# Kernel tuning notes

Measured on AMD Instinct MI355X. Metric: run time of the kernel, lower is better.

Reference implementation:

```python
import jax, jax.numpy as jnp
import numpy as np

N, E, D_IN, H, C, N_GRAPHS = 50000, 800000, 128, 2, 64, 50
D_HID = H * C  # 128
NEG_SLOPE = 0.2
EPS = 1e-16


def glorot(key, shape):
    fan_in, fan_out = shape[0], shape[-1]
    lim = jnp.sqrt(6.0 / (fan_in + fan_out))
    return jax.random.uniform(key, shape, jnp.float32, -lim, lim)


def setup_inputs() -> dict:
    key = jax.random.key(0)
    ks = jax.random.split(key, 12)
    x = jax.random.normal(ks[0], (N, D_IN), jnp.float32)
    edge_index = jax.random.randint(ks[1], (2, E), 0, N, jnp.int64)
    batch = jnp.sort(jax.random.randint(ks[2], (N,), 0, N_GRAPHS, jnp.int64))
    # GATConv layer 1: in=128 -> heads=2, out=64
    W1 = glorot(ks[3], (D_IN, H * C))
    as1 = glorot(ks[4], (1, H, C)).reshape(H, C)
    ad1 = glorot(ks[5], (1, H, C)).reshape(H, C)
    b1 = jnp.zeros((H * C,), jnp.float32)
    # GATConv layer 2: in=128 -> heads=2, out=64
    W2 = glorot(ks[6], (D_HID, H * C))
    as2 = glorot(ks[7], (1, H, C)).reshape(H, C)
    ad2 = glorot(ks[8], (1, H, C)).reshape(H, C)
    b2 = jnp.zeros((H * C,), jnp.float32)
    # Linear head: 128 -> 1
    Wh = glorot(ks[9], (D_HID, 1))
    bh = jnp.zeros((1,), jnp.float32)
    return {"x": x, "edge_index": edge_index, "batch": batch,
            "W1": W1, "as1": as1, "ad1": ad1, "b1": b1,
            "W2": W2, "as2": as2, "ad2": ad2, "b2": b2,
            "Wh": Wh, "bh": bh}


def gat_conv(x, src, dst, W, a_src, a_dst, bias):
    # PyG GATConv (concat=True, add_self_loops applied by caller, eval mode)
    n = x.shape[0]
    h = (x @ W).reshape(n, H, C)                       # [N,H,C]
    al_s = jnp.einsum('nhc,hc->nh', h, a_src)          # [N,H]
    al_d = jnp.einsum('nhc,hc->nh', h, a_dst)
    e = jax.nn.leaky_relu(al_s[src] + al_d[dst], NEG_SLOPE)  # [E',H]
    # segment softmax over incoming edges of each dst node
    e_max = jax.ops.segment_max(e, dst, num_segments=n)
    e = jnp.exp(e - e_max[dst])
    denom = jax.ops.segment_sum(e, dst, num_segments=n)
    alpha = e / (denom[dst] + EPS)                     # [E',H]
    out = jax.ops.segment_sum(alpha[:, :, None] * h[src], dst, num_segments=n)
    return out.reshape(n, H * C) + bias


def reference(x, edge_index, batch, W1, as1, ad1, b1, W2, as2, ad2, b2, Wh, bh):
    # add self-loops (PyG GATConv default)
    loops = jnp.arange(N, dtype=edge_index.dtype)
    src = jnp.concatenate([edge_index[0], loops])
    dst = jnp.concatenate([edge_index[1], loops])
    h = gat_conv(x, src, dst, W1, as1, ad1, b1)
    h = jax.nn.relu(h)  # dropout is identity in eval mode
    h = gat_conv(h, src, dst, W2, as2, ad2, b2)
    h = jax.nn.relu(h)
    # global mean pool over graphs
    sums = jax.ops.segment_sum(h, batch, num_segments=N_GRAPHS)
    counts = jax.ops.segment_sum(jnp.ones((N, 1), h.dtype), batch, num_segments=N_GRAPHS)
    pooled = sums / jnp.maximum(counts, 1.0)           # [G, 128]
    return pooled @ Wh + bh                            # [G, 1]
```

## Files before the change

### kernel.cpp

```cpp
#include <hip/hip_runtime.h>
#include <hip/hip_fp16.h>
#include <math.h>

#define HD 128
#define NEG_SLOPE 0.2f
#define EPSV 1e-16f
#define TILE 8192

typedef unsigned short ushort_t;
typedef __attribute__((ext_vector_type(8))) short bf16x8;
typedef __attribute__((ext_vector_type(4))) float f32x4;

__device__ inline void bsplit(float x, ushort_t& hi, ushort_t& lo) {
    unsigned u = __float_as_uint(x);
    unsigned hb = (u + 0x7FFFu + ((u >> 16) & 1u)) >> 16;
    hi = (ushort_t)hb;
    float res = x - __uint_as_float(hb << 16);
    unsigned v = __float_as_uint(res);
    lo = (ushort_t)((v + 0x7FFFu + ((v >> 16) & 1u)) >> 16);
}

__global__ __launch_bounds__(256) void part_hist(const int* __restrict__ dst,
                                                 int* __restrict__ tileHist, int E) {
    __shared__ int hist[256];
    int t = threadIdx.x;
    hist[t] = 0;
    __syncthreads();
    int base = blockIdx.x * TILE;
    int end = base + TILE; if (end > E) end = E;
    for (int i = base + t; i < end; i += 256)
        atomicAdd(&hist[dst[i] >> 8], 1);
    __syncthreads();
    tileHist[blockIdx.x * 256 + t] = hist[t];
}

__global__ __launch_bounds__(256) void part_offsets(int* __restrict__ tileHist,
                                                    int* __restrict__ bucketBase,
                                                    int NT) {
    __shared__ int s[256];
    int b = threadIdx.x;
    int total = 0;
    #pragma unroll 8
    for (int t = 0; t < NT; ++t) total += tileHist[t * 256 + b];
    s[b] = total;
    __syncthreads();
    for (int o = 1; o < 256; o <<= 1) {
        int v = (b >= o) ? s[b - o] : 0;
        __syncthreads();
        s[b] += v;
        __syncthreads();
    }
    int base = (b == 0) ? 0 : s[b - 1];
    bucketBase[b] = base;
    if (b == 255) bucketBase[256] = s[255];
    int run = base;
    #pragma unroll 8
    for (int t = 0; t < NT; ++t) {
        int v = tileHist[t * 256 + b];
        tileHist[t * 256 + b] = run;
        run += v;
    }
}

__global__ __launch_bounds__(256) void part_scatter(const int* __restrict__ src,
                                                    const int* __restrict__ dst,
                                                    const int* __restrict__ tileHist,
                                                    int2* __restrict__ part, int E) {
    __shared__ int cur[256];
    int t = threadIdx.x;
    cur[t] = tileHist[blockIdx.x * 256 + t];
    __syncthreads();
    int base = blockIdx.x * TILE;
    int end = base + TILE; if (end > E) end = E;
    for (int i = base + t; i < end; i += 256) {
        int d = dst[i], s = src[i];
        int p = atomicAdd(&cur[d >> 8], 1);
        part[p] = make_int2(s, d);
    }
}

__global__ __launch_bounds__(256) void fine_counts(const int2* __restrict__ part,
                                                   const int* __restrict__ bucketBase,
                                                   int* __restrict__ cnt, int N) {
    __shared__ int hist[256];
    int t = threadIdx.x;
    hist[t] = 0;
    __syncthreads();
    int b = blockIdx.x;
    int s0 = bucketBase[b], s1 = bucketBase[b + 1];
    for (int i = s0 + t; i < s1; i += 256)
        atomicAdd(&hist[part[i].y & 255], 1);
    __syncthreads();
    int d = b * 256 + t;
    if (d < N) cnt[d] = hist[t] + 1;
}

__global__ __launch_bounds__(256) void block_sums(const int* __restrict__ cnt,
                                                  int* __restrict__ bsum, int N) {
    __shared__ int s[4];
    int t = threadIdx.x;
    int i = blockIdx.x * 256 + t;
    int v = (i < N) ? cnt[i] : 0;
    for (int o = 32; o >= 1; o >>= 1) v += __shfl_xor(v, o, 64);
    if ((t & 63) == 0) s[t >> 6] = v;
    __syncthreads();
    if (t == 0) bsum[blockIdx.x] = s[0] + s[1] + s[2] + s[3];
}

__global__ __launch_bounds__(256) void scan_bsums(int* __restrict__ bsum, int NB) {
    __shared__ int s[256];
    __shared__ int carry;
    int t = threadIdx.x;
    if (t == 0) carry = 0;
    __syncthreads();
    for (int base = 0; base < NB; base += 256) {
        int i = base + t;
        int v = (i < NB) ? bsum[i] : 0;
        s[t] = v;
        __syncthreads();
        for (int o = 1; o < 256; o <<= 1) {
            int u = (t >= o) ? s[t - o] : 0;
            __syncthreads();
            s[t] += u;
            __syncthreads();
        }
        int excl = ((t == 0) ? 0 : s[t - 1]) + carry;
        if (i < NB) bsum[i] = excl;
        __syncthreads();
        if (t == 0) carry += s[255];
        __syncthreads();
    }
}

__global__ __launch_bounds__(256) void scatter_scan(const int* __restrict__ cnt,
                                                    const int* __restrict__ bsum,
                                                    int* __restrict__ indptr, int N) {
    __shared__ int s[256];
    int t = threadIdx.x;
    int i = blockIdx.x * 256 + t;
    int v = (i < N) ? cnt[i] : 0;
    s[t] = v;
    __syncthreads();
    for (int o = 1; o < 256; o <<= 1) {
        int u = (t >= o) ? s[t - o] : 0;
        __syncthreads();
        s[t] += u;
        __syncthreads();
    }
    int excl = ((t == 0) ? 0 : s[t - 1]) + bsum[blockIdx.x];
    if (i < N) indptr[i] = excl;
    if (i == N - 1) indptr[N] = excl + v;
}

__global__ __launch_bounds__(256) void csr_scatter(const int2* __restrict__ part,
                                                   const int* __restrict__ bucketBase,
                                                   const int* __restrict__ indptr,
                                                   int* __restrict__ csr, int N) {
    __shared__ int cur[256];
    int t = threadIdx.x;
    int b = blockIdx.x;
    int d = b * 256 + t;
    cur[t] = (d < N) ? indptr[d] : 0;
    __syncthreads();
    int s0 = bucketBase[b], s1 = bucketBase[b + 1];
    for (int i = s0 + t; i < s1; i += 256) {
        int2 e = part[i];
        int p = atomicAdd(&cur[e.y & 255], 1);
        csr[p] = e.x;
    }
    __syncthreads();
    if (d < N) csr[cur[t]] = d;
}

__global__ __launch_bounds__(256) void split_w(const float* __restrict__ W,
                                               ushort_t* __restrict__ Whs,
                                               ushort_t* __restrict__ Wls) {
    int idx = blockIdx.x * 256 + threadIdx.x;
    int j    = idx & 7;
    int lane = (idx >> 3) & 63;
    int ks   = (idx >> 9) & 3;
    int ct   = idx >> 11;
    int n = ct * 16 + (lane & 15);
    int k = ks * 32 + (lane >> 4) * 8 + j;
    ushort_t hi, lo;
    bsplit(W[k * 128 + n], hi, lo);
    Whs[idx] = hi;
    Wls[idx] = lo;
}

__device__ inline void load8(const float* p, float* vv) {
    float4 a = *(const float4*)p;
    float4 b = *(const float4*)(p + 4);
    vv[0]=a.x; vv[1]=a.y; vv[2]=a.z; vv[3]=a.w;
    vv[4]=b.x; vv[5]=b.y; vv[6]=b.z; vv[7]=b.w;
}
__device__ inline void load8(const __half* p, float* vv) {
    bf16x8 r = *(const bf16x8*)p;
    #pragma unroll
    for (int j = 0; j < 8; ++j)
        vv[j] = __half2float(__ushort_as_half((ushort_t)r[j]));
}

template <typename TA>
__global__ __launch_bounds__(256) void gemm_mfma(const TA* __restrict__ A,
                                                 const ushort_t* __restrict__ Whs,
                                                 const ushort_t* __restrict__ Wls,
                                                 const float* __restrict__ a_s,
                                                 const float* __restrict__ a_d,
                                                 __half* __restrict__ h16,
                                                 float* __restrict__ als,
                                                 float* __restrict__ ald, int N) {
    const int gw   = (blockIdx.x * 256 + threadIdx.x) >> 6;
    const int lane = threadIdx.x & 63;
    const int r0   = gw * 16;
    if (r0 >= N) return;
    const int m = lane & 15;
    const int q = lane >> 4;

    bf16x8 ah[4], al[4];
    {
        int row = r0 + m;
        if (row >= N) row = N - 1;
        const TA* ap = A + (size_t)row * HD;
        #pragma unroll
        for (int ks = 0; ks < 4; ++ks) {
            float vv[8];
            load8(ap + ks * 32 + q * 8, vv);
            #pragma unroll
            for (int j = 0; j < 8; ++j) {
                ushort_t hb, lb;
                bsplit(vv[j], hb, lb);
                ah[ks][j] = (short)hb;
                al[ks][j] = (short)lb;
            }
        }
    }

    float ps[4] = {0,0,0,0};
    float pd[4] = {0,0,0,0};

    #pragma unroll 1
    for (int ct = 0; ct < 8; ++ct) {
        f32x4 acc = {0.f, 0.f, 0.f, 0.f};
        #pragma unroll
        for (int ks = 0; ks < 4; ++ks) {
            bf16x8 wh = *(const bf16x8*)(Whs + ((size_t)(ct * 4 + ks) * 64 + lane) * 8);
            bf16x8 wl = *(const bf16x8*)(Wls + ((size_t)(ct * 4 + ks) * 64 + lane) * 8);
            acc = __builtin_amdgcn_mfma_f32_16x16x32_bf16(ah[ks], wh, acc, 0, 0, 0);
            acc = __builtin_amdgcn_mfma_f32_16x16x32_bf16(al[ks], wh, acc, 0, 0, 0);
            acc = __builtin_amdgcn_mfma_f32_16x16x32_bf16(ah[ks], wl, acc, 0, 0, 0);
        }
        const int col = ct * 16 + m;
        const float asv = a_s[col], adv = a_d[col];
        #pragma unroll
        for (int reg = 0; reg < 4; ++reg) {
            ps[reg] += acc[reg] * asv;
            pd[reg] += acc[reg] * adv;
            int row = r0 + q * 4 + reg;
            if (row < N) h16[(size_t)row * HD + col] = __float2half(acc[reg]);
        }
        if (ct == 3 || ct == 7) {
            int head = ct >> 2;
            #pragma unroll
            for (int reg = 0; reg < 4; ++reg) {
                float vs = ps[reg], vd = pd[reg];
                for (int o = 8; o >= 1; o >>= 1) {
                    vs += __shfl_xor(vs, o, 64);
                    vd += __shfl_xor(vd, o, 64);
                }
                if (m == 0) {
                    int row = r0 + q * 4 + reg;
                    if (row < N) { als[2 * row + head] = vs; ald[2 * row + head] = vd; }
                }
                ps[reg] = 0.f;  pd[reg] = 0.f;
            }
        }
    }
}

__global__ __launch_bounds__(256) void gat_aggregate(const __half* __restrict__ h,
                                                     const float* __restrict__ als,
                                                     const float* __restrict__ ald,
                                                     const int* __restrict__ indptr,
                                                     const int* __restrict__ csr,
                                                     const float* __restrict__ bias,
                                                     __half* __restrict__ out,
                                                     const float* __restrict__ Wh,
                                                     float* __restrict__ svec, int N) {
    int w    = (blockIdx.x * blockDim.x + threadIdx.x) >> 6;
    int lane = threadIdx.x & 63;
    if (w >= N) return;
    int start = indptr[w], end = indptr[w + 1];
    float ad0 = ald[2 * w], ad1 = ald[2 * w + 1];
    const bool head0 = (lane < 32);
    const int cbase = lane * 2;

    float accx = 0.f, accy = 0.f, d0 = 0.f, d1 = 0.f;
    for (int base = start; base < end; base += 64) {
        int i = base + lane;
        int idx = i < end ? i : end - 1;
        int s = csr[idx];
        unsigned wpack = 0u;
        if (i < end) {
            float2 av = *(const float2*)&als[2 * s];
            float e0 = av.x + ad0;
            float e1 = av.y + ad1;
            e0 = e0 > 0.f ? e0 : NEG_SLOPE * e0;
            e1 = e1 > 0.f ? e1 : NEG_SLOPE * e1;
            __half p0 = __float2half(__expf(e0));
            __half p1 = __float2half(__expf(e1));
            wpack = ((unsigned)__half_as_ushort(p1) << 16) | __half_as_ushort(p0);
            d0 += __half2float(p0);
            d1 += __half2float(p1);
        }
        int nl = end - base; if (nl > 64) nl = 64;
        int nb = (nl + 7) >> 3;
        for (int b = 0; b < nb; ++b) {
            int j = b * 8;
            int sj[8]; float wa[8];
            #pragma unroll
            for (int u = 0; u < 8; ++u) {
                sj[u] = __shfl(s, j + u, 64);
                unsigned wp = (unsigned)__shfl((int)wpack, j + u, 64);
                unsigned bits = head0 ? (wp & 0xffffu) : (wp >> 16);
                wa[u] = __half2float(__ushort_as_half((ushort_t)bits));
            }
            __half2 hv[8];
            #pragma unroll
            for (int u = 0; u < 8; ++u)
                hv[u] = *(const __half2*)&h[(size_t)sj[u] * HD + cbase];
            #pragma unroll
            for (int u = 0; u < 8; ++u) {
                float2 f = __half22float2(hv[u]);
                accx += wa[u] * f.x;
                accy += wa[u] * f.y;
            }
        }
    }
    for (int o = 32; o >= 1; o >>= 1) {
        d0 += __shfl_xor(d0, o, 64);
        d1 += __shfl_xor(d1, o, 64);
    }
    float D = (head0 ? d0 : d1) + EPSV;
    float ox = accx / D + bias[cbase];
    float oy = accy / D + bias[cbase + 1];
    ox = ox > 0.f ? ox : 0.f;
    oy = oy > 0.f ? oy : 0.f;

    if (svec) {
        float2 wv = *(const float2*)&Wh[cbase];
        float part = ox * wv.x + oy * wv.y;
        for (int o = 32; o >= 1; o >>= 1) part += __shfl_xor(part, o, 64);
        if (lane == 0) svec[w] = part;
    } else {
        *(__half2*)&out[(size_t)w * HD + cbase] =
            __halves2half2(__float2half(ox), __float2half(oy));
    }
}

__global__ void graph_bounds(const int* __restrict__ batch, int* __restrict__ gstart,
                             int N, int G) {
    int g = blockIdx.x * blockDim.x + threadIdx.x;
    if (g > G) return;
    int lo = 0, hi = N;
    while (lo < hi) {
        int mid = (lo + hi) >> 1;
        if (batch[mid] < g) lo = mid + 1; else hi = mid;
    }
    gstart[g] = lo;
}

__global__ __launch_bounds__(256) void pool_reduce(const float* __restrict__ s,
                                                   const int* __restrict__ gstart,
                                                   const float* __restrict__ bh,
                                                   float* __restrict__ out, int G) {
    __shared__ float partial[4];
    int g = blockIdx.x, t = threadIdx.x;
    int a = gstart[g], b = gstart[g + 1];
    float sum = 0.f;
    for (int i = a + t; i < b; i += 256) sum += s[i];
    for (int o = 32; o >= 1; o >>= 1) sum += __shfl_xor(sum, o, 64);
    if ((t & 63) == 0) partial[t >> 6] = sum;
    __syncthreads();
    if (t == 0) {
        float cnt = (float)(b - a); if (cnt < 1.f) cnt = 1.f;
        out[g] = (partial[0] + partial[1] + partial[2] + partial[3]) / cnt + bh[0];
    }
}

extern "C" void kernel_launch(void* const* d_in, const int* in_sizes, int n_in,
                              void* d_out, int out_size, void* d_ws, size_t ws_size,
                              hipStream_t stream) {
    const float* x     = (const float*)d_in[0];
    const int*   ei    = (const int*)d_in[1];
    const int*   batch = (const int*)d_in[2];
    const float* W1  = (const float*)d_in[3];
    const float* as1 = (const float*)d_in[4];
    const float* ad1 = (const float*)d_in[5];
    const float* b1  = (const float*)d_in[6];
    const float* W2  = (const float*)d_in[7];
    const float* as2 = (const float*)d_in[8];
    const float* ad2 = (const float*)d_in[9];
    const float* b2  = (const float*)d_in[10];
    const float* Wh  = (const float*)d_in[11];
    const float* bh  = (const float*)d_in[12];
    float* out = (float*)d_out;

    const int N = in_sizes[0] / HD;
    const int E = in_sizes[1] / 2;
    const int G = out_size;
    const int* srcp = ei;
    const int* dstp = ei + E;
    const int NB  = (N + 255) / 256;
    const int NBK = (N + 255) / 256;
    const int NT  = (E + TILE - 1) / TILE;

    char* ws = (char*)d_ws;
    size_t off = 0;
    auto alloc = [&](size_t bytes) -> void* {
        void* p = ws + off;
        off += (bytes + 255) & ~(size_t)255;
        return p;
    };
    __half* h16   = (__half*)alloc((size_t)N * HD * 2);
    __half* ob16  = (__half*)alloc((size_t)N * HD * 2);
    float* als    = (float*)alloc((size_t)N * 2 * 4);
    float* ald    = (float*)alloc((size_t)N * 2 * 4);
    float* svec   = (float*)alloc((size_t)N * 4);
    int*   indptr = (int*)  alloc((size_t)(N + 1) * 4);
    int*   cnt    = (int*)  alloc((size_t)N * 4);
    int*   bsum   = (int*)  alloc((size_t)NB * 4);
    int*   csr    = (int*)  alloc((size_t)(E + N) * 4);
    int*   gstart = (int*)  alloc((size_t)(G + 1) * 4);
    int*   tileHist   = (int*)alloc((size_t)NT * 256 * 4);
    int*   bucketBase = (int*)alloc(257 * 4);
    int2*  part   = (int2*) alloc((size_t)E * 8);
    ushort_t* Whs1 = (ushort_t*)alloc(16384 * 2);
    ushort_t* Wls1 = (ushort_t*)alloc(16384 * 2);
    ushort_t* Whs2 = (ushort_t*)alloc(16384 * 2);
    ushort_t* Wls2 = (ushort_t*)alloc(16384 * 2);

    part_hist<<<NT, 256, 0, stream>>>(dstp, tileHist, E);
    part_offsets<<<1, 256, 0, stream>>>(tileHist, bucketBase, NT);
    part_scatter<<<NT, 256, 0, stream>>>(srcp, dstp, tileHist, part, E);
    fine_counts<<<NBK, 256, 0, stream>>>(part, bucketBase, cnt, N);
    block_sums<<<NB, 256, 0, stream>>>(cnt, bsum, N);
    scan_bsums<<<1, 256, 0, stream>>>(bsum, NB);
    scatter_scan<<<NB, 256, 0, stream>>>(cnt, bsum, indptr, N);
    csr_scatter<<<NBK, 256, 0, stream>>>(part, bucketBase, indptr, csr, N);
    graph_bounds<<<1, 64, 0, stream>>>(batch, gstart, N, G);

    split_w<<<64, 256, 0, stream>>>(W1, Whs1, Wls1);
    split_w<<<64, 256, 0, stream>>>(W2, Whs2, Wls2);

    const int nwaves  = (N + 15) / 16;
    const int gblocks = (nwaves + 3) / 4;
    int wgrid = (N * 64 + 255) / 256;

    gemm_mfma<<<gblocks, 256, 0, stream>>>(x, Whs1, Wls1, as1, ad1, h16, als, ald, N);
    gat_aggregate<<<wgrid, 256, 0, stream>>>(h16, als, ald, indptr, csr, b1, ob16,
                                             nullptr, nullptr, N);
    gemm_mfma<<<gblocks, 256, 0, stream>>>(ob16, Whs2, Wls2, as2, ad2, h16, als, ald, N);
    gat_aggregate<<<wgrid, 256, 0, stream>>>(h16, als, ald, indptr, csr, b2, nullptr,
                                             Wh, svec, N);
    pool_reduce<<<G, 256, 0, stream>>>(svec, gstart, bh, out, G);
}
```

Measured before the change: 264.0 us.

## Pack partition entries, fuse CSR scan kernels, double-buffer aggregate gathers

Partition entries are packed into a single int (src<<8 | low dst byte) instead of an int2, halving partition traffic. Block sums are computed directly in fine_counts from bucket sizes, and the local scan is fused into csr_scatter, removing two kernel launches. The aggregate inner loop is software-pipelined with two register buffers so the next group's gathers are issued before the current group is accumulated. The packing assumes src < 2^23, and the double buffer raises register pressure.

```diff
diff --git a/kernel.cpp b/kernel.cpp
--- a/kernel.cpp
+++ b/kernel.cpp
@@ -65,7 +65,7 @@
 __global__ __launch_bounds__(256) void part_scatter(const int* __restrict__ src,
                                                     const int* __restrict__ dst,
                                                     const int* __restrict__ tileHist,
-                                                    int2* __restrict__ part, int E) {
+                                                    int* __restrict__ part, int E) {
     __shared__ int cur[256];
     int t = threadIdx.x;
     cur[t] = tileHist[blockIdx.x * 256 + t];
@@ -75,13 +75,14 @@
     for (int i = base + t; i < end; i += 256) {
         int d = dst[i], s = src[i];
         int p = atomicAdd(&cur[d >> 8], 1);
-        part[p] = make_int2(s, d);
-    }
-}
-
-__global__ __launch_bounds__(256) void fine_counts(const int2* __restrict__ part,
+        part[p] = (s << 8) | (d & 255);
+    }
+}
+
+__global__ __launch_bounds__(256) void fine_counts(const int* __restrict__ part,
                                                    const int* __restrict__ bucketBase,
-                                                   int* __restrict__ cnt, int N) {
+                                                   int* __restrict__ cnt,
+                                                   int* __restrict__ bsum, int N) {
     __shared__ int hist[256];
     int t = threadIdx.x;
     hist[t] = 0;
@@ -89,22 +90,14 @@
     int b = blockIdx.x;
     int s0 = bucketBase[b], s1 = bucketBase[b + 1];
     for (int i = s0 + t; i < s1; i += 256)
-        atomicAdd(&hist[part[i].y & 255], 1);
+        atomicAdd(&hist[part[i] & 255], 1);
     __syncthreads();
     int d = b * 256 + t;
     if (d < N) cnt[d] = hist[t] + 1;
-}
-
-__global__ __launch_bounds__(256) void block_sums(const int* __restrict__ cnt,
-                                                  int* __restrict__ bsum, int N) {
-    __shared__ int s[4];
-    int t = threadIdx.x;
-    int i = blockIdx.x * 256 + t;
-    int v = (i < N) ? cnt[i] : 0;
-    for (int o = 32; o >= 1; o >>= 1) v += __shfl_xor(v, o, 64);
-    if ((t & 63) == 0) s[t >> 6] = v;
-    __syncthreads();
-    if (t == 0) bsum[blockIdx.x] = s[0] + s[1] + s[2] + s[3];
+    if (t == 0) {
+        int nn = N - b * 256; if (nn > 256) nn = 256; if (nn < 0) nn = 0;
+        bsum[b] = (s1 - s0) + nn;
+    }
 }
 
 __global__ __launch_bounds__(256) void scan_bsums(int* __restrict__ bsum, int NB) {
@@ -132,41 +125,36 @@
     }
 }
 
-__global__ __launch_bounds__(256) void scatter_scan(const int* __restrict__ cnt,
-                                                    const int* __restrict__ bsum,
-                                                    int* __restrict__ indptr, int N) {
+__global__ __launch_bounds__(256) void csr_scatter(const int* __restrict__ part,
+                                                   const int* __restrict__ bucketBase,
+                                                   const int* __restrict__ cnt,
+                                                   const int* __restrict__ bsum,
+                                                   int* __restrict__ indptr,
+                                                   int* __restrict__ csr, int N) {
     __shared__ int s[256];
-    int t = threadIdx.x;
-    int i = blockIdx.x * 256 + t;
-    int v = (i < N) ? cnt[i] : 0;
-    s[t] = v;
-    __syncthreads();
-    for (int o = 1; o < 256; o <<= 1) {
-        int u = (t >= o) ? s[t - o] : 0;
-        __syncthreads();
-        s[t] += u;
-        __syncthreads();
-    }
-    int excl = ((t == 0) ? 0 : s[t - 1]) + bsum[blockIdx.x];
-    if (i < N) indptr[i] = excl;
-    if (i == N - 1) indptr[N] = excl + v;
-}
-
-__global__ __launch_bounds__(256) void csr_scatter(const int2* __restrict__ part,
-                                                   const int* __restrict__ bucketBase,
-                                                   const int* __restrict__ indptr,
-                                                   int* __restrict__ csr, int N) {
     __shared__ int cur[256];
     int t = threadIdx.x;
     int b = blockIdx.x;
     int d = b * 256 + t;
-    cur[t] = (d < N) ? indptr[d] : 0;
+    int v = (d < N) ? cnt[d] : 0;
+    s[t] = v;
+    __syncthreads();
+    for (int o = 1; o < 256; o <<= 1) {
+        int u = (t >= o) ? s[t - o] : 0;
+        __syncthreads();
+        s[t] += u;
+        __syncthreads();
+    }
+    int excl = ((t == 0) ? 0 : s[t - 1]) + bsum[b];
+    if (d < N) indptr[d] = excl;
+    if (d == N - 1) indptr[N] = excl + v;
+    cur[t] = excl;
     __syncthreads();
     int s0 = bucketBase[b], s1 = bucketBase[b + 1];
     for (int i = s0 + t; i < s1; i += 256) {
-        int2 e = part[i];
-        int p = atomicAdd(&cur[e.y & 255], 1);
-        csr[p] = e.x;
+        int e = part[i];
+        int p = atomicAdd(&cur[e & 255], 1);
+        csr[p] = e >> 8;
     }
     __syncthreads();
     if (d < N) csr[cur[t]] = d;
@@ -315,9 +303,12 @@
         }
         int nl = end - base; if (nl > 64) nl = 64;
         int nb = (nl + 7) >> 3;
-        for (int b = 0; b < nb; ++b) {
-            int j = b * 8;
-            int sj[8]; float wa[8];
+
+        float waA[8], waB[8];
+        __half2 hvA[8], hvB[8];
+
+        auto fetch = [&](int j, float* wa, __half2* hv) {
+            int sj[8];
             #pragma unroll
             for (int u = 0; u < 8; ++u) {
                 sj[u] = __shfl(s, j + u, 64);
@@ -325,17 +316,26 @@
                 unsigned bits = head0 ? (wp & 0xffffu) : (wp >> 16);
                 wa[u] = __half2float(__ushort_as_half((ushort_t)bits));
             }
-            __half2 hv[8];
             #pragma unroll
             for (int u = 0; u < 8; ++u)
                 hv[u] = *(const __half2*)&h[(size_t)sj[u] * HD + cbase];
+        };
+        auto consume = [&](const float* wa, const __half2* hv) {
             #pragma unroll
             for (int u = 0; u < 8; ++u) {
                 float2 f = __half22float2(hv[u]);
                 accx += wa[u] * f.x;
                 accy += wa[u] * f.y;
             }
-        }
+        };
+
+        fetch(0, waA, hvA);
+        int b = 0;
+        for (; b + 1 < nb; ++b) {
+            if (b & 1) { fetch((b + 1) * 8, waA, hvA); consume(waB, hvB); }
+            else       { fetch((b + 1) * 8, waB, hvB); consume(waA, hvA); }
+        }
+        if (b & 1) consume(waB, hvB); else consume(waA, hvA);
     }
     for (int o = 32; o >= 1; o >>= 1) {
         d0 += __shfl_xor(d0, o, 64);
@@ -411,7 +411,6 @@
     const int G = out_size;
     const int* srcp = ei;
     const int* dstp = ei + E;
-    const int NB  = (N + 255) / 256;
     const int NBK = (N + 255) / 256;
     const int NT  = (E + TILE - 1) / TILE;
 
@@ -429,12 +428,12 @@
     float* svec   = (float*)alloc((size_t)N * 4);
     int*   indptr = (int*)  alloc((size_t)(N + 1) * 4);
     int*   cnt    = (int*)  alloc((size_t)N * 4);
-    int*   bsum   = (int*)  alloc((size_t)NB * 4);
+    int*   bsum   = (int*)  alloc((size_t)NBK * 4);
     int*   csr    = (int*)  alloc((size_t)(E + N) * 4);
     int*   gstart = (int*)  alloc((size_t)(G + 1) * 4);
     int*   tileHist   = (int*)alloc((size_t)NT * 256 * 4);
     int*   bucketBase = (int*)alloc(257 * 4);
-    int2*  part   = (int2*) alloc((size_t)E * 8);
+    int*   part   = (int*)  alloc((size_t)E * 4);
     ushort_t* Whs1 = (ushort_t*)alloc(16384 * 2);
     ushort_t* Wls1 = (ushort_t*)alloc(16384 * 2);
     ushort_t* Whs2 = (ushort_t*)alloc(16384 * 2);
@@ -443,11 +442,9 @@
     part_hist<<<NT, 256, 0, stream>>>(dstp, tileHist, E);
     part_offsets<<<1, 256, 0, stream>>>(tileHist, bucketBase, NT);
     part_scatter<<<NT, 256, 0, stream>>>(srcp, dstp, tileHist, part, E);
-    fine_counts<<<NBK, 256, 0, stream>>>(part, bucketBase, cnt, N);
-    block_sums<<<NB, 256, 0, stream>>>(cnt, bsum, N);
-    scan_bsums<<<1, 256, 0, stream>>>(bsum, NB);
-    scatter_scan<<<NB, 256, 0, stream>>>(cnt, bsum, indptr, N);
-    csr_scatter<<<NBK, 256, 0, stream>>>(part, bucketBase, indptr, csr, N);
+    fine_counts<<<NBK, 256, 0, stream>>>(part, bucketBase, cnt, bsum, N);
+    scan_bsums<<<1, 256, 0, stream>>>(bsum, NBK);
+    csr_scatter<<<NBK, 256, 0, stream>>>(part, bucketBase, cnt, bsum, indptr, csr, N);
     graph_bounds<<<1, 64, 0, stream>>>(batch, gstart, N, G);
 
     split_w<<<64, 256, 0, stream>>>(W1, Whs1, Wls1);
```

Measured after the change: 276.4 us. +4.7%, slower.
